# Kernel tuning notes

Measured on AMD Instinct MI355X. Metric: run time of the kernel, lower is better.

## Reference

```python
import jax, jax.numpy as jnp
import numpy as np

K = 1024
D = 64
N = 262144

def setup_inputs() -> dict:
    key = jax.random.key(0)
    k1, k2 = jax.random.split(key)
    z_e = jax.random.normal(k1, (N, D), dtype=jnp.float32)
    # nn.Embedding weight init: uniform(-1/K, 1/K)
    codebook = jax.random.uniform(k2, (K, D), dtype=jnp.float32, minval=-1.0 / K, maxval=1.0 / K)
    return {"z_e": z_e, "codebook": codebook}

def reference(z_e, codebook):
    # torch.cdist -> Euclidean distances; argmin over squared distances is identical
    # and avoids the sqrt. dist2[n,k] = ||z_e[n]||^2 - 2 z_e@cb^T + ||cb[k]||^2
    ze_sq = jnp.sum(z_e * z_e, axis=1, keepdims=True)            # [N,1]
    cb_sq = jnp.sum(codebook * codebook, axis=1)                  # [K]
    dist2 = ze_sq - 2.0 * (z_e @ codebook.T) + cb_sq[None, :]     # [N,K]
    encoding_inds = jnp.argmin(dist2, axis=1)                     # [N]
    z_q = codebook[encoding_inds]                                 # [N,D] gather
    return (z_q, encoding_inds)
```

## Files before the change

kernel.cpp:

```cpp
#include <hip/hip_runtime.h>


#define VQ_D 64
#define VQ_MAXK 1024

#define VQ_CH2(qa, qb, c) do { \
    s0 = fmaf((qa).x, (c).x, s0); s1 = fmaf((qb).x, (c).x, s1); \
    s0 = fmaf((qa).y, (c).y, s0); s1 = fmaf((qb).y, (c).y, s1); \
    s0 = fmaf((qa).z, (c).z, s0); s1 = fmaf((qb).z, (c).z, s1); \
    s0 = fmaf((qa).w, (c).w, s0); s1 = fmaf((qb).w, (c).w, s1); } while (0)

#define VQ_SQ(acc, q) do { \
    (acc) += (double)(q).x * (double)(q).x; \
    (acc) += (double)(q).y * (double)(q).y; \
    (acc) += (double)(q).z * (double)(q).z; \
    (acc) += (double)(q).w * (double)(q).w; } while (0)

__global__ __launch_bounds__(256, 2) void vq_argmin_kernel(
    const float* __restrict__ z_e,
    const float* __restrict__ cb,
    float* __restrict__ out,
    int N, int K)
{
    __shared__ float s_cbsq[VQ_MAXK];

    for (int k = threadIdx.x; k < K; k += blockDim.x) {
        const float* c = cb + (size_t)k * VQ_D;
        double s = 0.0;
        #pragma unroll
        for (int d = 0; d < VQ_D; ++d) { double v = (double)c[d]; s += v * v; }
        s_cbsq[k] = (float)s;
    }
    __syncthreads();

    int n0 = blockIdx.x * (2 * blockDim.x) + threadIdx.x;
    if (n0 >= N) return;
    int n1 = n0 + blockDim.x;
    if (n1 >= N) n1 = n0;

    const float4* zp0 = (const float4*)(z_e + (size_t)n0 * VQ_D);
    const float4* zp1 = (const float4*)(z_e + (size_t)n1 * VQ_D);
    float4 a0  = zp0[0],  a1  = zp0[1],  a2  = zp0[2],  a3  = zp0[3];
    float4 a4  = zp0[4],  a5  = zp0[5],  a6  = zp0[6],  a7  = zp0[7];
    float4 a8  = zp0[8],  a9  = zp0[9],  a10 = zp0[10], a11 = zp0[11];
    float4 a12 = zp0[12], a13 = zp0[13], a14 = zp0[14], a15 = zp0[15];
    float4 b0  = zp1[0],  b1  = zp1[1],  b2  = zp1[2],  b3  = zp1[3];
    float4 b4  = zp1[4],  b5  = zp1[5],  b6  = zp1[6],  b7  = zp1[7];
    float4 b8  = zp1[8],  b9  = zp1[9],  b10 = zp1[10], b11 = zp1[11];
    float4 b12 = zp1[12], b13 = zp1[13], b14 = zp1[14], b15 = zp1[15];

    double zs0 = 0.0, zs1 = 0.0;
    VQ_SQ(zs0, a0);  VQ_SQ(zs0, a1);  VQ_SQ(zs0, a2);  VQ_SQ(zs0, a3);
    VQ_SQ(zs0, a4);  VQ_SQ(zs0, a5);  VQ_SQ(zs0, a6);  VQ_SQ(zs0, a7);
    VQ_SQ(zs0, a8);  VQ_SQ(zs0, a9);  VQ_SQ(zs0, a10); VQ_SQ(zs0, a11);
    VQ_SQ(zs0, a12); VQ_SQ(zs0, a13); VQ_SQ(zs0, a14); VQ_SQ(zs0, a15);
    VQ_SQ(zs1, b0);  VQ_SQ(zs1, b1);  VQ_SQ(zs1, b2);  VQ_SQ(zs1, b3);
    VQ_SQ(zs1, b4);  VQ_SQ(zs1, b5);  VQ_SQ(zs1, b6);  VQ_SQ(zs1, b7);
    VQ_SQ(zs1, b8);  VQ_SQ(zs1, b9);  VQ_SQ(zs1, b10); VQ_SQ(zs1, b11);
    VQ_SQ(zs1, b12); VQ_SQ(zs1, b13); VQ_SQ(zs1, b14); VQ_SQ(zs1, b15);
    const float zsq0 = (float)zs0;
    const float zsq1 = (float)zs1;

    float best0 = 3.4e38f, best1 = 3.4e38f;
    int bk0 = 0, bk1 = 0;

    #pragma unroll 1
    for (int k = 0; k < K; ++k) {
        const float4* __restrict__ cp = (const float4*)(cb + (size_t)k * VQ_D);
        float4 c0  = cp[0],  c1  = cp[1],  c2  = cp[2],  c3  = cp[3];
        float4 c4  = cp[4],  c5  = cp[5],  c6  = cp[6],  c7  = cp[7];
        float4 c8  = cp[8],  c9  = cp[9],  c10 = cp[10], c11 = cp[11];
        float4 c12 = cp[12], c13 = cp[13], c14 = cp[14], c15 = cp[15];

        float s0 = 0.f, s1 = 0.f;
        VQ_CH2(a0,  b0,  c0);  VQ_CH2(a1,  b1,  c1);
        VQ_CH2(a2,  b2,  c2);  VQ_CH2(a3,  b3,  c3);
        VQ_CH2(a4,  b4,  c4);  VQ_CH2(a5,  b5,  c5);
        VQ_CH2(a6,  b6,  c6);  VQ_CH2(a7,  b7,  c7);
        VQ_CH2(a8,  b8,  c8);  VQ_CH2(a9,  b9,  c9);
        VQ_CH2(a10, b10, c10); VQ_CH2(a11, b11, c11);
        VQ_CH2(a12, b12, c12); VQ_CH2(a13, b13, c13);
        VQ_CH2(a14, b14, c14); VQ_CH2(a15, b15, c15);

        const float cq = s_cbsq[k];
        const float u0    = zsq0 - 2.0f * s0;
        const float dist0 = u0 + cq;
        const float u1    = zsq1 - 2.0f * s1;
        const float dist1 = u1 + cq;
        if (dist0 < best0) { best0 = dist0; bk0 = k; }
        if (dist1 < best1) { best1 = dist1; bk1 = k; }
    }

    {
        const float4* cq0 = (const float4*)(cb + (size_t)bk0 * VQ_D);
        float4* oq0 = (float4*)(out + (size_t)n0 * VQ_D);
        #pragma unroll
        for (int i = 0; i < VQ_D / 4; ++i) oq0[i] = cq0[i];
        const float4* cq1 = (const float4*)(cb + (size_t)bk1 * VQ_D);
        float4* oq1 = (float4*)(out + (size_t)n1 * VQ_D);
        #pragma unroll
        for (int i = 0; i < VQ_D / 4; ++i) oq1[i] = cq1[i];
    }

    out[(size_t)N * VQ_D + n0] = (float)bk0;
    out[(size_t)N * VQ_D + n1] = (float)bk1;
}

extern "C" void kernel_launch(void* const* d_in, const int* in_sizes, int n_in,
                              void* d_out, int out_size, void* d_ws, size_t ws_size,
                              hipStream_t stream) {
    const float* z_e = (const float*)d_in[0];
    const float* cb  = (const float*)d_in[1];
    float* out = (float*)d_out;

    const int N = in_sizes[0] / VQ_D;
    const int K = in_sizes[1] / VQ_D;

    const int block = 256;
    const int rows_per_block = 2 * block;
    const int grid = (N + rows_per_block - 1) / rows_per_block;
    vq_argmin_kernel<<<grid, block, 0, stream>>>(z_e, cb, out, N, K);
}
```

Baseline: 615.6 us.

## Stage codebook tiles in shared memory with double-buffered prefetch

Replaces per-thread direct global reads of each codebook row with cooperative loading of 64-row tiles into LDS, double-buffered so the next tile's global load overlaps compute on the current one. Threads past N are clamped rather than returning early so every thread reaches the barriers, and the writes are guarded instead. This adds a block barrier per tile and LDS read traffic, and it may displace what were previously wave-uniform scalar/cached loads.

```diff
diff --git a/kernel.cpp b/kernel.cpp
--- a/kernel.cpp
+++ b/kernel.cpp
@@ -3,6 +3,8 @@
 
 #define VQ_D 64
 #define VQ_MAXK 1024
+#define TILE_ROWS 64
+#define TILE_F4 (TILE_ROWS * (VQ_D / 4))
 
 #define VQ_CH2(qa, qb, c) do { \
     s0 = fmaf((qa).x, (c).x, s0); s1 = fmaf((qb).x, (c).x, s1); \
@@ -22,21 +24,25 @@
     float* __restrict__ out,
     int N, int K)
 {
-    __shared__ float s_cbsq[VQ_MAXK];
+    __shared__ float  s_cbsq[VQ_MAXK];
+    __shared__ float4 s_tile[2][TILE_F4];
 
-    for (int k = threadIdx.x; k < K; k += blockDim.x) {
+    const int tid = threadIdx.x;
+
+    for (int k = tid; k < K; k += blockDim.x) {
         const float* c = cb + (size_t)k * VQ_D;
         double s = 0.0;
         #pragma unroll
         for (int d = 0; d < VQ_D; ++d) { double v = (double)c[d]; s += v * v; }
         s_cbsq[k] = (float)s;
     }
-    __syncthreads();
 
-    int n0 = blockIdx.x * (2 * blockDim.x) + threadIdx.x;
-    if (n0 >= N) return;
-    int n1 = n0 + blockDim.x;
-    if (n1 >= N) n1 = n0;
+    int n0 = blockIdx.x * (2 * (int)blockDim.x) + tid;
+    const bool v0 = (n0 < N);
+    if (!v0) n0 = N - 1;
+    int n1 = n0 + (int)blockDim.x;
+    const bool v1 = (n1 < N);
+    if (!v1) n1 = n0;
 
     const float4* zp0 = (const float4*)(z_e + (size_t)n0 * VQ_D);
     const float4* zp1 = (const float4*)(z_e + (size_t)n1 * VQ_D);
@@ -61,49 +67,80 @@
     const float zsq0 = (float)zs0;
     const float zsq1 = (float)zs1;
 
+    const float4* cb4 = (const float4*)cb;
+    {
+        float4 t0 = cb4[tid],       t1 = cb4[tid + 256];
+        float4 t2 = cb4[tid + 512], t3 = cb4[tid + 768];
+        s_tile[0][tid]       = t0;  s_tile[0][tid + 256] = t1;
+        s_tile[0][tid + 512] = t2;  s_tile[0][tid + 768] = t3;
+    }
+    __syncthreads();
+
     float best0 = 3.4e38f, best1 = 3.4e38f;
     int bk0 = 0, bk1 = 0;
 
+    const int NT = K / TILE_ROWS;
+    int cur = 0;
+
     #pragma unroll 1
-    for (int k = 0; k < K; ++k) {
-        const float4* __restrict__ cp = (const float4*)(cb + (size_t)k * VQ_D);
-        float4 c0  = cp[0],  c1  = cp[1],  c2  = cp[2],  c3  = cp[3];
-        float4 c4  = cp[4],  c5  = cp[5],  c6  = cp[6],  c7  = cp[7];
-        float4 c8  = cp[8],  c9  = cp[9],  c10 = cp[10], c11 = cp[11];
-        float4 c12 = cp[12], c13 = cp[13], c14 = cp[14], c15 = cp[15];
+    for (int t = 0; t < NT; ++t) {
+        const int tn = (t + 1 < NT) ? (t + 1) : t;
+        const float4* gp = cb4 + (size_t)tn * TILE_F4;
+        float4 t0 = gp[tid],       t1 = gp[tid + 256];
+        float4 t2 = gp[tid + 512], t3 = gp[tid + 768];
 
-        float s0 = 0.f, s1 = 0.f;
-        VQ_CH2(a0,  b0,  c0);  VQ_CH2(a1,  b1,  c1);
-        VQ_CH2(a2,  b2,  c2);  VQ_CH2(a3,  b3,  c3);
-        VQ_CH2(a4,  b4,  c4);  VQ_CH2(a5,  b5,  c5);
-        VQ_CH2(a6,  b6,  c6);  VQ_CH2(a7,  b7,  c7);
-        VQ_CH2(a8,  b8,  c8);  VQ_CH2(a9,  b9,  c9);
-        VQ_CH2(a10, b10, c10); VQ_CH2(a11, b11, c11);
-        VQ_CH2(a12, b12, c12); VQ_CH2(a13, b13, c13);
-        VQ_CH2(a14, b14, c14); VQ_CH2(a15, b15, c15);
+        const float4* lt = &s_tile[cur][0];
+        const int kbase = t * TILE_ROWS;
 
-        const float cq = s_cbsq[k];
-        const float u0    = zsq0 - 2.0f * s0;
-        const float dist0 = u0 + cq;
-        const float u1    = zsq1 - 2.0f * s1;
-        const float dist1 = u1 + cq;
-        if (dist0 < best0) { best0 = dist0; bk0 = k; }
-        if (dist1 < best1) { best1 = dist1; bk1 = k; }
+        #pragma unroll 1
+        for (int r = 0; r < TILE_ROWS; ++r) {
+            const float4* rp = lt + (r << 4);
+            float s0 = 0.f, s1 = 0.f;
+
+            float4 c0 = rp[0], c1 = rp[1], c2 = rp[2], c3 = rp[3];
+            float4 c4 = rp[4], c5 = rp[5], c6 = rp[6], c7 = rp[7];
+            VQ_CH2(a0, b0, c0); VQ_CH2(a1, b1, c1);
+            VQ_CH2(a2, b2, c2); VQ_CH2(a3, b3, c3);
+            VQ_CH2(a4, b4, c4); VQ_CH2(a5, b5, c5);
+            VQ_CH2(a6, b6, c6); VQ_CH2(a7, b7, c7);
+
+            float4 d0 = rp[8],  d1 = rp[9],  d2 = rp[10], d3 = rp[11];
+            float4 d4 = rp[12], d5 = rp[13], d6 = rp[14], d7 = rp[15];
+            VQ_CH2(a8,  b8,  d0); VQ_CH2(a9,  b9,  d1);
+            VQ_CH2(a10, b10, d2); VQ_CH2(a11, b11, d3);
+            VQ_CH2(a12, b12, d4); VQ_CH2(a13, b13, d5);
+            VQ_CH2(a14, b14, d6); VQ_CH2(a15, b15, d7);
+
+            const int k = kbase + r;
+            const float cq = s_cbsq[k];
+            const float u0    = zsq0 - 2.0f * s0;
+            const float dist0 = u0 + cq;
+            const float u1    = zsq1 - 2.0f * s1;
+            const float dist1 = u1 + cq;
+            if (dist0 < best0) { best0 = dist0; bk0 = k; }
+            if (dist1 < best1) { best1 = dist1; bk1 = k; }
+        }
+
+        s_tile[cur ^ 1][tid]       = t0;  s_tile[cur ^ 1][tid + 256] = t1;
+        s_tile[cur ^ 1][tid + 512] = t2;  s_tile[cur ^ 1][tid + 768] = t3;
+        __syncthreads();
+        cur ^= 1;
     }
 
-    {
+    if (v0) {
         const float4* cq0 = (const float4*)(cb + (size_t)bk0 * VQ_D);
         float4* oq0 = (float4*)(out + (size_t)n0 * VQ_D);
         #pragma unroll
         for (int i = 0; i < VQ_D / 4; ++i) oq0[i] = cq0[i];
+        out[(size_t)N * VQ_D + n0] = (float)bk0;
+    }
+    if (v1) {
         const float4* cq1 = (const float4*)(cb + (size_t)bk1 * VQ_D);
         float4* oq1 = (float4*)(out + (size_t)n1 * VQ_D);
         #pragma unroll
         for (int i = 0; i < VQ_D / 4; ++i) oq1[i] = cq1[i];
+        out[(size_t)N * VQ_D + n1] = (float)bk1;
     }
-
-    out[(size_t)N * VQ_D + n0] = (float)bk0;
-    out[(size_t)N * VQ_D + n1] = (float)bk1;
 }
 
 extern "C" void kernel_launch(void* const* d_in, const int* in_sizes, int n_in,
```

Measured after the change: 586.7 us. 4.7% less time.

## Software-pipeline codebook loads via constant address space and precompute norms

Applied to the files above, without the earlier changes.

Codebook rows are now read through the constant address space (address_space(4)), which allows scalar loads because every thread reads the same row. The loop is double-buffered: the next row's first half is fetched while the current row's second half is used, with sched barriers to pin the order. Codebook squared norms move to a separate small kernel that writes into the workspace, which removes the per-block norm computation and its __syncthreads. The cost is an extra kernel launch and reliance on the workspace being present.

```diff
diff --git a/kernel.cpp b/kernel.cpp
--- a/kernel.cpp
+++ b/kernel.cpp
@@ -3,6 +3,10 @@
 
 #define VQ_D 64
 #define VQ_MAXK 1024
+
+typedef __attribute__((ext_vector_type(4))) float f4;
+typedef const __attribute__((address_space(4))) f4* cb4c_t;
+typedef const __attribute__((address_space(4))) float* fc_t;
 
 #define VQ_CH2(qa, qb, c) do { \
     s0 = fmaf((qa).x, (c).x, s0); s1 = fmaf((qb).x, (c).x, s1); \
@@ -16,26 +20,44 @@
     (acc) += (double)(q).z * (double)(q).z; \
     (acc) += (double)(q).w * (double)(q).w; } while (0)
 
+#define SBAR() __builtin_amdgcn_sched_barrier(0)
+
+__global__ void vq_cbsq_kernel(const float* __restrict__ cb,
+                               float* __restrict__ cbsq, int K)
+{
+    const int k = blockIdx.x * blockDim.x + threadIdx.x;
+    if (k >= K) return;
+    const float* c = cb + (size_t)k * VQ_D;
+    double s = 0.0;
+    #pragma unroll
+    for (int d = 0; d < VQ_D; ++d) { double v = (double)c[d]; s += v * v; }
+    cbsq[k] = (float)s;
+}
+
+template <bool USE_WS>
 __global__ __launch_bounds__(256, 2) void vq_argmin_kernel(
     const float* __restrict__ z_e,
     const float* __restrict__ cb,
+    const float* __restrict__ cbsq_ws,
     float* __restrict__ out,
     int N, int K)
 {
     __shared__ float s_cbsq[VQ_MAXK];
 
-    for (int k = threadIdx.x; k < K; k += blockDim.x) {
-        const float* c = cb + (size_t)k * VQ_D;
-        double s = 0.0;
-        #pragma unroll
-        for (int d = 0; d < VQ_D; ++d) { double v = (double)c[d]; s += v * v; }
-        s_cbsq[k] = (float)s;
+    if (!USE_WS) {
+        for (int k = threadIdx.x; k < K; k += blockDim.x) {
+            const float* c = cb + (size_t)k * VQ_D;
+            double s = 0.0;
+            #pragma unroll
+            for (int d = 0; d < VQ_D; ++d) { double v = (double)c[d]; s += v * v; }
+            s_cbsq[k] = (float)s;
+        }
+        __syncthreads();
     }
-    __syncthreads();
 
-    int n0 = blockIdx.x * (2 * blockDim.x) + threadIdx.x;
+    int n0 = blockIdx.x * (2 * (int)blockDim.x) + threadIdx.x;
     if (n0 >= N) return;
-    int n1 = n0 + blockDim.x;
+    int n1 = n0 + (int)blockDim.x;
     if (n1 >= N) n1 = n0;
 
     const float4* zp0 = (const float4*)(z_e + (size_t)n0 * VQ_D);
@@ -61,28 +83,47 @@
     const float zsq0 = (float)zs0;
     const float zsq1 = (float)zs1;
 
+    cb4c_t cbc = (cb4c_t)(unsigned long long)cb;
+    fc_t   sqc = (fc_t)(unsigned long long)cbsq_ws;
+
     float best0 = 3.4e38f, best1 = 3.4e38f;
     int bk0 = 0, bk1 = 0;
 
+    f4 X0, X1, X2, X3, X4, X5, X6, X7;
+    f4 Y0, Y1, Y2, Y3, Y4, Y5, Y6, Y7;
+    float cq;
+
+    X0 = cbc[0]; X1 = cbc[1]; X2 = cbc[2]; X3 = cbc[3];
+    X4 = cbc[4]; X5 = cbc[5]; X6 = cbc[6]; X7 = cbc[7];
+
     #pragma unroll 1
     for (int k = 0; k < K; ++k) {
-        const float4* __restrict__ cp = (const float4*)(cb + (size_t)k * VQ_D);
-        float4 c0  = cp[0],  c1  = cp[1],  c2  = cp[2],  c3  = cp[3];
-        float4 c4  = cp[4],  c5  = cp[5],  c6  = cp[6],  c7  = cp[7];
-        float4 c8  = cp[8],  c9  = cp[9],  c10 = cp[10], c11 = cp[11];
-        float4 c12 = cp[12], c13 = cp[13], c14 = cp[14], c15 = cp[15];
+        const int kb = k << 4;
+        float s0 = 0.f, s1 = 0.f;
 
-        float s0 = 0.f, s1 = 0.f;
-        VQ_CH2(a0,  b0,  c0);  VQ_CH2(a1,  b1,  c1);
-        VQ_CH2(a2,  b2,  c2);  VQ_CH2(a3,  b3,  c3);
-        VQ_CH2(a4,  b4,  c4);  VQ_CH2(a5,  b5,  c5);
-        VQ_CH2(a6,  b6,  c6);  VQ_CH2(a7,  b7,  c7);
-        VQ_CH2(a8,  b8,  c8);  VQ_CH2(a9,  b9,  c9);
-        VQ_CH2(a10, b10, c10); VQ_CH2(a11, b11, c11);
-        VQ_CH2(a12, b12, c12); VQ_CH2(a13, b13, c13);
-        VQ_CH2(a14, b14, c14); VQ_CH2(a15, b15, c15);
+        VQ_CH2(a0, b0, X0);
+        SBAR();
+        Y0 = cbc[kb + 8];  Y1 = cbc[kb + 9];  Y2 = cbc[kb + 10]; Y3 = cbc[kb + 11];
+        Y4 = cbc[kb + 12]; Y5 = cbc[kb + 13]; Y6 = cbc[kb + 14]; Y7 = cbc[kb + 15];
+        cq = USE_WS ? sqc[k] : s_cbsq[k];
+        SBAR();
+        VQ_CH2(a1, b1, X1); VQ_CH2(a2, b2, X2); VQ_CH2(a3, b3, X3);
+        VQ_CH2(a4, b4, X4); VQ_CH2(a5, b5, X5); VQ_CH2(a6, b6, X6);
+        VQ_CH2(a7, b7, X7);
 
-        const float cq = s_cbsq[k];
+        VQ_CH2(a8, b8, Y0);
+        SBAR();
+        {
+            int nk = k + 1; if (nk >= K) nk = K - 1;
+            const int nb = nk << 4;
+            X0 = cbc[nb + 0]; X1 = cbc[nb + 1]; X2 = cbc[nb + 2]; X3 = cbc[nb + 3];
+            X4 = cbc[nb + 4]; X5 = cbc[nb + 5]; X6 = cbc[nb + 6]; X7 = cbc[nb + 7];
+        }
+        SBAR();
+        VQ_CH2(a9,  b9,  Y1); VQ_CH2(a10, b10, Y2); VQ_CH2(a11, b11, Y3);
+        VQ_CH2(a12, b12, Y4); VQ_CH2(a13, b13, Y5); VQ_CH2(a14, b14, Y6);
+        VQ_CH2(a15, b15, Y7);
+
         const float u0    = zsq0 - 2.0f * s0;
         const float dist0 = u0 + cq;
         const float u1    = zsq1 - 2.0f * s1;
@@ -119,5 +160,13 @@
     const int block = 256;
     const int rows_per_block = 2 * block;
     const int grid = (N + rows_per_block - 1) / rows_per_block;
-    vq_argmin_kernel<<<grid, block, 0, stream>>>(z_e, cb, out, N, K);
+
+    const bool use_ws = (d_ws != nullptr) && (ws_size >= (size_t)K * sizeof(float));
+    if (use_ws) {
+        float* cbsq = (float*)d_ws;
+        vq_cbsq_kernel<<<(K + 255) / 256, 256, 0, stream>>>(cb, cbsq, K);
+        vq_argmin_kernel<true><<<grid, block, 0, stream>>>(z_e, cb, cbsq, out, N, K);
+    } else {
+        vq_argmin_kernel<false><<<grid, block, 0, stream>>>(z_e, cb, nullptr, out, N, K);
+    }
 }
```

Result: faster. 584.1 us (-5.1%).
